# Kernel optimization log

Measured on AMD Instinct MI355X. Metric: run time of the kernel, lower is better.

Reference implementation:

```python
import jax, jax.numpy as jnp
import numpy as np

TEMPERATURE = 0.1
NORMALIZED = True


def _l2norm(x, eps=1e-12):
    # matches F.normalize(p=2, dim=1)
    n = jnp.sqrt(jnp.sum(x * x, axis=1, keepdims=True))
    return x / jnp.maximum(n, eps)


def setup_inputs() -> dict:
    key = jax.random.key(0)
    k1, k2, k3, k4 = jax.random.split(key, 4)
    B, D = 4096, 256
    return {
        "hs": jax.random.normal(k1, (B, D), dtype=jnp.float32),
        "ht0": jax.random.normal(k2, (B, D), dtype=jnp.float32),
        "ht1": jax.random.normal(k3, (B, D), dtype=jnp.float32),
        "labels": jax.random.randint(k4, (B,), 0, 100, dtype=jnp.int64)
        if jax.config.jax_enable_x64 else jax.random.randint(k4, (B,), 0, 100, dtype=jnp.int32),
        "num_views": 2,
    }


def _per_teacher_loss(hs_n, ht_n, mask, logits_mask, batch_size, num_views):
    # features: [N, D] with N = 2B
    features = jnp.concatenate([hs_n, ht_n], axis=0)
    sim = jnp.matmul(features, features.T) / TEMPERATURE          # [N, N]
    exp_logits = jnp.exp(sim) * logits_mask                        # [N, N]
    log_prob = sim - jnp.log(jnp.sum(exp_logits, axis=1, keepdims=True))
    per_inst = -jnp.sum(mask * log_prob, axis=1) / jnp.sum(mask, axis=1)  # [N]
    if num_views > 1:
        per_inst = per_inst.reshape(batch_size, num_views).mean(axis=1)
    return per_inst.mean()


def reference(hs, ht0, ht1, labels, num_views):
    batch_size = labels.shape[0]
    hs = hs.reshape(batch_size, -1)
    ht_list = [ht0.reshape(batch_size, -1), ht1.reshape(batch_size, -1)]
    if NORMALIZED:
        hs = _l2norm(hs)
        ht_list = [_l2norm(ht) for ht in ht_list]

    labels2 = jnp.concatenate([labels, labels])                    # [N]
    mask = (labels2[:, None] == labels2[None, :]).astype(jnp.float32)
    N = 2 * batch_size
    logits_mask = 1.0 - jnp.eye(N, dtype=jnp.float32)              # zero diagonal
    mask = mask * logits_mask

    inter_loss = 0.0
    for ht in ht_list:
        inter_loss = inter_loss + _per_teacher_loss(
            hs, ht, mask, logits_mask, batch_size, num_views)
    return inter_loss / len(ht_list)
```

## Files before the change

### kernel.cpp

```cpp
#include <hip/hip_runtime.h>
#include <hip/hip_bf16.h>

#define B_SIZE 4096
#define D_SIZE 256
#define N_SIZE 8192
#define NCHUNK 8
#define CHUNK (N_SIZE / NCHUNK)
#define GROUP 64
#define NGROUPS (CHUNK / GROUP)

typedef __attribute__((ext_vector_type(8))) short short8;
typedef __attribute__((ext_vector_type(4))) float floatx4;


__device__ __forceinline__ void async16(void* lds, const void* g) {
    __builtin_amdgcn_global_load_lds(
        (const __attribute__((address_space(1))) unsigned int*)g,
        (__attribute__((address_space(3))) unsigned int*)lds, 16, 0, 0);
}
__device__ __forceinline__ void async4(void* lds, const void* g) {
    __builtin_amdgcn_global_load_lds(
        (const __attribute__((address_space(1))) unsigned int*)g,
        (__attribute__((address_space(3))) unsigned int*)lds, 4, 0, 0);
}

__global__ void norm_kernel(const float* __restrict__ hs,
                            const float* __restrict__ ht0,
                            const float* __restrict__ ht1,
                            __hip_bfloat16* __restrict__ dst,
                            float* __restrict__ zero_region) {
    int id  = blockIdx.x;
    int tid = threadIdx.x;
    int gid = id * 256 + tid;
    if (gid < 2 * 2 * N_SIZE) zero_region[gid] = 0.0f;

    const float* src = (id < 4096) ? (hs + id * D_SIZE)
                     : (id < 8192) ? (ht0 + (id - 4096) * D_SIZE)
                                   : (ht1 + (id - 8192) * D_SIZE);
    float x = src[tid];
    float ss = x * x;
#pragma unroll
    for (int off = 32; off > 0; off >>= 1) ss += __shfl_xor(ss, off);
    __shared__ float wsum[4];
    int wave = tid >> 6, lane = tid & 63;
    if (lane == 0) wsum[wave] = ss;
    __syncthreads();
    float tot = wsum[0] + wsum[1] + wsum[2] + wsum[3];
    float inv = 1.0f / fmaxf(sqrtf(tot), 1e-12f);
    dst[id * D_SIZE + tid] = __float2bfloat16(x * inv);
}

__global__ __launch_bounds__(256)
void sim_kernel(const __hip_bfloat16* __restrict__ featS,
                const __hip_bfloat16* __restrict__ featT0,
                const __hip_bfloat16* __restrict__ featT1,
                const int* __restrict__ labels,
                float* __restrict__ Sarr,
                float* __restrict__ Aarr) {
    __shared__ __align__(16) unsigned char sB[2][32768];
    __shared__ int sLab[2][GROUP];

    const int rb    = blockIdx.x;
    const int t     = blockIdx.y;
    const int chunk = blockIdx.z;
    const __hip_bfloat16* featT = t ? featT1 : featT0;

    const int tid  = threadIdx.x;
    const int w    = tid >> 6;
    const int l    = tid & 63;
    const int quad = l >> 4;
    const int lcol = l & 15;
    const int row_base = rb * 128 + w * 32;

    short8 af[2][8];
#pragma unroll
    for (int rt = 0; rt < 2; ++rt) {
        int arow = row_base + rt * 16 + lcol;
        const __hip_bfloat16* ap = (arow < B_SIZE) ? featS + arow * D_SIZE
                                                   : featT + (arow - B_SIZE) * D_SIZE;
#pragma unroll
        for (int ks = 0; ks < 8; ++ks)
            af[rt][ks] = *reinterpret_cast<const short8*>(ap + ks * 32 + quad * 8);
    }

    int labr[2][4];
#pragma unroll
    for (int rt = 0; rt < 2; ++rt)
#pragma unroll
        for (int r = 0; r < 4; ++r)
            labr[rt][r] = labels[(row_base + rt * 16 + quad * 4 + r) & (B_SIZE - 1)];

    float Sp[2][4] = {{0.f,0.f,0.f,0.f},{0.f,0.f,0.f,0.f}};
    float Ap[2][4] = {{0.f,0.f,0.f,0.f},{0.f,0.f,0.f,0.f}};

    const int col0 = chunk * CHUNK;

    auto stage = [&](int b, int cb) {
#pragma unroll
        for (int i = 0; i < 8; ++i) {
            int cl  = i * 2 + (l >> 5);
            int c   = (l & 31) ^ (cl & 7);
            int col = cb + w * 16 + cl;
            const __hip_bfloat16* cp = (col < B_SIZE) ? featS + col * D_SIZE
                                                      : featT + (col - B_SIZE) * D_SIZE;
            async16(&sB[b][w * 8192 + i * 1024], (const char*)cp + c * 16);
        }
        if (w == 0) async4(&sLab[b][0], &labels[(cb + l) & (B_SIZE - 1)]);
    };

    stage(0, col0);

    for (int g = 0; g < NGROUPS; ++g) {
        const int buf = g & 1;
        const int cb  = col0 + g * GROUP;
        __syncthreads();
        if (g + 1 < NGROUPS) stage(buf ^ 1, cb + GROUP);

        floatx4 acc[4][2];
#pragma unroll
        for (int u = 0; u < 4; ++u)
#pragma unroll
            for (int rt = 0; rt < 2; ++rt)
                acc[u][rt] = floatx4{0.f, 0.f, 0.f, 0.f};

#pragma unroll
        for (int ks = 0; ks < 8; ++ks) {
            short8 bf[4];
#pragma unroll
            for (int u = 0; u < 4; ++u)
                bf[u] = *reinterpret_cast<const short8*>(
                    &sB[buf][u * 8192 + lcol * 512 + ((ks * 4 + quad) ^ (lcol & 7)) * 16]);
#pragma unroll
            for (int u = 0; u < 4; ++u)
#pragma unroll
                for (int rt = 0; rt < 2; ++rt)
                    acc[u][rt] = __builtin_amdgcn_mfma_f32_16x16x32_bf16(
                        af[rt][ks], bf[u], acc[u][rt], 0, 0, 0);
        }

#pragma unroll
        for (int u = 0; u < 4; ++u) {
            const int bcol = cb + u * 16 + lcol;
            const int labj = sLab[buf][u * 16 + lcol];
#pragma unroll
            for (int rt = 0; rt < 2; ++rt)
#pragma unroll
                for (int r = 0; r < 4; ++r) {
                    const int row = row_base + rt * 16 + quad * 4 + r;
                    const float a = acc[u][rt][r];
                    const float e = __expf(a * 10.0f);
                    const bool diag = (row == bcol);
                    Sp[rt][r] += diag ? 0.f : e;
                    Ap[rt][r] += (!diag && labj == labr[rt][r]) ? a : 0.f;
                }
        }
    }

#pragma unroll
    for (int rt = 0; rt < 2; ++rt)
#pragma unroll
        for (int r = 0; r < 4; ++r) {
#pragma unroll
            for (int m = 1; m < 16; m <<= 1) {
                Sp[rt][r] += __shfl_xor(Sp[rt][r], m);
                Ap[rt][r] += __shfl_xor(Ap[rt][r], m);
            }
        }
    if (lcol == 0) {
#pragma unroll
        for (int rt = 0; rt < 2; ++rt)
#pragma unroll
            for (int r = 0; r < 4; ++r) {
                const int row = row_base + rt * 16 + quad * 4 + r;
                atomicAdd(&Sarr[t * N_SIZE + row], Sp[rt][r]);
                atomicAdd(&Aarr[t * N_SIZE + row], Ap[rt][r]);
            }
    }
}

__global__ void final_kernel(const float* __restrict__ Sarr,
                             const float* __restrict__ Aarr,
                             const int* __restrict__ labels,
                             float* __restrict__ out) {
    __shared__ int h[128];
    __shared__ float wsum[16];
    int tid = threadIdx.x;
    if (tid < 128) h[tid] = 0;
    __syncthreads();
    for (int i = tid; i < B_SIZE; i += 1024) atomicAdd(&h[labels[i] & 127], 1);
    __syncthreads();
    float acc = 0.f;
    for (int idx = tid; idx < 2 * N_SIZE; idx += 1024) {
        int i = idx & (N_SIZE - 1);
        float M = 2.0f * (float)h[labels[i & (B_SIZE - 1)] & 127] - 1.0f;
        acc += logf(Sarr[idx]) - 10.0f * Aarr[idx] / M;
    }
#pragma unroll
    for (int off = 32; off > 0; off >>= 1) acc += __shfl_xor(acc, off);
    int wv = tid >> 6, ln = tid & 63;
    if (ln == 0) wsum[wv] = acc;
    __syncthreads();
    if (tid == 0) {
        float tot = 0.f;
#pragma unroll
        for (int k = 0; k < 16; ++k) tot += wsum[k];
        out[0] = tot / 16384.0f;
    }
}

extern "C" void kernel_launch(void* const* d_in, const int* in_sizes, int n_in,
                              void* d_out, int out_size, void* d_ws, size_t ws_size,
                              hipStream_t stream) {
    const float* hs     = (const float*)d_in[0];
    const float* ht0    = (const float*)d_in[1];
    const float* ht1    = (const float*)d_in[2];
    const int*   labels = (const int*)d_in[3];

    char* ws = (char*)d_ws;
    float* Sarr = (float*)(ws);
    float* Aarr = (float*)(ws + 65536);
    __hip_bfloat16* featS  = (__hip_bfloat16*)(ws + 131072);
    __hip_bfloat16* featT0 = (__hip_bfloat16*)(ws + 131072 + 2097152);
    __hip_bfloat16* featT1 = (__hip_bfloat16*)(ws + 131072 + 2 * 2097152);

    norm_kernel<<<3 * 4096, 256, 0, stream>>>(hs, ht0, ht1, featS, Sarr);
    sim_kernel<<<dim3(64, 2, NCHUNK), 256, 0, stream>>>(featS, featT0, featT1, labels, Sarr, Aarr);
    final_kernel<<<1, 1024, 0, stream>>>(Sarr, Aarr, labels, (float*)d_out);
}
```

Baseline: 170.2 us.

## Compute positive-pair sums via per-label centroids and drop masking from sim loop

The sim kernel no longer evaluates label and diagonal masks per element. It sums exp over all columns, and a new rowstat kernel subtracts the diagonal term exp(10*|f_i|^2). The masked positive-logit sum is rewritten algebraically as a dot product of each row with per-label feature sums, which a new gvec kernel accumulates with atomics. The sim tile also grows to 64 rows per wave with fewer blocks (launch bounds 2), the LDS layout drops the swizzle, and the final reduction becomes a multi-block ticket pattern. Risks include precision loss from subtracting the diagonal exp out of S, bank conflicts from the unswizzled LDS reads, and the serial per-block gvec reduction.

After: 304.4 us. 1.79x slower.

```diff
diff --git a/kernel.cpp b/kernel.cpp
--- a/kernel.cpp
+++ b/kernel.cpp
@@ -5,11 +5,13 @@
 #define D_SIZE 256
 #define N_SIZE 8192
 #define NCHUNK 8
-#define CHUNK (N_SIZE / NCHUNK)
+#define CHUNK 1024
 #define GROUP 64
 #define NGROUPS (CHUNK / GROUP)
+#define LOG2E10 14.4269504089f
 
 typedef __attribute__((ext_vector_type(8))) short short8;
+typedef __attribute__((ext_vector_type(4))) short short4v;
 typedef __attribute__((ext_vector_type(4))) float floatx4;
 
 
@@ -17,11 +19,6 @@
     __builtin_amdgcn_global_load_lds(
         (const __attribute__((address_space(1))) unsigned int*)g,
         (__attribute__((address_space(3))) unsigned int*)lds, 16, 0, 0);
-}
-__device__ __forceinline__ void async4(void* lds, const void* g) {
-    __builtin_amdgcn_global_load_lds(
-        (const __attribute__((address_space(1))) unsigned int*)g,
-        (__attribute__((address_space(3))) unsigned int*)lds, 4, 0, 0);
 }
 
 __global__ void norm_kernel(const float* __restrict__ hs,
@@ -32,7 +29,7 @@
     int id  = blockIdx.x;
     int tid = threadIdx.x;
     int gid = id * 256 + tid;
-    if (gid < 2 * 2 * N_SIZE) zero_region[gid] = 0.0f;
+    if (gid < 114818) zero_region[gid] = 0.0f;
 
     const float* src = (id < 4096) ? (hs + id * D_SIZE)
                      : (id < 8192) ? (ht0 + (id - 4096) * D_SIZE)
@@ -50,15 +47,44 @@
     dst[id * D_SIZE + tid] = __float2bfloat16(x * inv);
 }
 
-__global__ __launch_bounds__(256)
+__global__ void gvec_kernel(const __hip_bfloat16* __restrict__ featBase,
+                            const int* __restrict__ labels,
+                            float* __restrict__ gOut,
+                            int* __restrict__ cnt) {
+    __shared__ float lg[64 * 256];
+    __shared__ int slab[256];
+    const int b   = blockIdx.x;
+    const int tid = threadIdx.x;
+    const int set = b >> 4;
+    const int rs0 = (b & 15) * 256;
+    const __hip_bfloat16* f = featBase + set * B_SIZE * D_SIZE;
+    float* gset = gOut + set * 32768;
+
+    slab[tid] = labels[rs0 + tid] & 127;
+    __syncthreads();
+    if (set == 0) atomicAdd(&cnt[slab[tid]], 1);
+
+    for (int pass = 0; pass < 2; ++pass) {
+        for (int k = 0; k < 64; ++k) lg[k * 256 + tid] = 0.0f;
+        __syncthreads();
+        for (int it = 0; it < 256; ++it) {
+            int lab = slab[it];
+            if ((lab >> 6) == pass)
+                lg[(lab & 63) * 256 + tid] += __bfloat162float(f[(rs0 + it) * D_SIZE + tid]);
+        }
+        __syncthreads();
+        for (int k = 0; k < 64; ++k)
+            atomicAdd(&gset[pass * 16384 + k * 256 + tid], lg[k * 256 + tid]);
+        __syncthreads();
+    }
+}
+
+__global__ __launch_bounds__(256, 2)
 void sim_kernel(const __hip_bfloat16* __restrict__ featS,
                 const __hip_bfloat16* __restrict__ featT0,
                 const __hip_bfloat16* __restrict__ featT1,
-                const int* __restrict__ labels,
-                float* __restrict__ Sarr,
-                float* __restrict__ Aarr) {
+                float* __restrict__ Sarr) {
     __shared__ __align__(16) unsigned char sB[2][32768];
-    __shared__ int sLab[2][GROUP];
 
     const int rb    = blockIdx.x;
     const int t     = blockIdx.y;
@@ -70,11 +96,11 @@
     const int l    = tid & 63;
     const int quad = l >> 4;
     const int lcol = l & 15;
-    const int row_base = rb * 128 + w * 32;
-
-    short8 af[2][8];
-#pragma unroll
-    for (int rt = 0; rt < 2; ++rt) {
+    const int row_base = rb * 256 + w * 64;
+
+    short8 af[4][8];
+#pragma unroll
+    for (int rt = 0; rt < 4; ++rt) {
         int arow = row_base + rt * 16 + lcol;
         const __hip_bfloat16* ap = (arow < B_SIZE) ? featS + arow * D_SIZE
                                                    : featT + (arow - B_SIZE) * D_SIZE;
@@ -83,128 +109,142 @@
             af[rt][ks] = *reinterpret_cast<const short8*>(ap + ks * 32 + quad * 8);
     }
 
-    int labr[2][4];
-#pragma unroll
-    for (int rt = 0; rt < 2; ++rt)
-#pragma unroll
-        for (int r = 0; r < 4; ++r)
-            labr[rt][r] = labels[(row_base + rt * 16 + quad * 4 + r) & (B_SIZE - 1)];
-
-    float Sp[2][4] = {{0.f,0.f,0.f,0.f},{0.f,0.f,0.f,0.f}};
-    float Ap[2][4] = {{0.f,0.f,0.f,0.f},{0.f,0.f,0.f,0.f}};
+    float Sp[4][4];
+#pragma unroll
+    for (int rt = 0; rt < 4; ++rt)
+#pragma unroll
+        for (int r = 0; r < 4; ++r) Sp[rt][r] = 0.0f;
 
     const int col0 = chunk * CHUNK;
 
     auto stage = [&](int b, int cb) {
-#pragma unroll
-        for (int i = 0; i < 8; ++i) {
-            int cl  = i * 2 + (l >> 5);
-            int c   = (l & 31) ^ (cl & 7);
-            int col = cb + w * 16 + cl;
-            const __hip_bfloat16* cp = (col < B_SIZE) ? featS + col * D_SIZE
-                                                      : featT + (col - B_SIZE) * D_SIZE;
-            async16(&sB[b][w * 8192 + i * 1024], (const char*)cp + c * 16);
-        }
-        if (w == 0) async4(&sLab[b][0], &labels[(cb + l) & (B_SIZE - 1)]);
+        int tb = cb + w * 16;
+        const __hip_bfloat16* cp = (tb < B_SIZE) ? featS + tb * D_SIZE
+                                                 : featT + (tb - B_SIZE) * D_SIZE;
+        const char* gp = (const char*)cp + (l & 15) * 512 + (l >> 4) * 16;
+        unsigned char* lp = &sB[b][w * 8192];
+#pragma unroll
+        for (int ks = 0; ks < 8; ++ks)
+            async16(lp + ks * 1024, gp + ks * 64);
     };
 
     stage(0, col0);
 
     for (int g = 0; g < NGROUPS; ++g) {
         const int buf = g & 1;
-        const int cb  = col0 + g * GROUP;
-        __syncthreads();
-        if (g + 1 < NGROUPS) stage(buf ^ 1, cb + GROUP);
-
-        floatx4 acc[4][2];
-#pragma unroll
-        for (int u = 0; u < 4; ++u)
-#pragma unroll
-            for (int rt = 0; rt < 2; ++rt)
-                acc[u][rt] = floatx4{0.f, 0.f, 0.f, 0.f};
-
-#pragma unroll
-        for (int ks = 0; ks < 8; ++ks) {
-            short8 bf[4];
-#pragma unroll
-            for (int u = 0; u < 4; ++u)
-                bf[u] = *reinterpret_cast<const short8*>(
-                    &sB[buf][u * 8192 + lcol * 512 + ((ks * 4 + quad) ^ (lcol & 7)) * 16]);
-#pragma unroll
-            for (int u = 0; u < 4; ++u)
-#pragma unroll
-                for (int rt = 0; rt < 2; ++rt)
-                    acc[u][rt] = __builtin_amdgcn_mfma_f32_16x16x32_bf16(
-                        af[rt][ks], bf[u], acc[u][rt], 0, 0, 0);
-        }
-
-#pragma unroll
-        for (int u = 0; u < 4; ++u) {
-            const int bcol = cb + u * 16 + lcol;
-            const int labj = sLab[buf][u * 16 + lcol];
-#pragma unroll
-            for (int rt = 0; rt < 2; ++rt)
-#pragma unroll
-                for (int r = 0; r < 4; ++r) {
-                    const int row = row_base + rt * 16 + quad * 4 + r;
-                    const float a = acc[u][rt][r];
-                    const float e = __expf(a * 10.0f);
-                    const bool diag = (row == bcol);
-                    Sp[rt][r] += diag ? 0.f : e;
-                    Ap[rt][r] += (!diag && labj == labr[rt][r]) ? a : 0.f;
-                }
-        }
-    }
-
-#pragma unroll
-    for (int rt = 0; rt < 2; ++rt)
+        __syncthreads();
+        if (g + 1 < NGROUPS) stage(buf ^ 1, col0 + (g + 1) * GROUP);
+
+#pragma unroll
+        for (int up = 0; up < 2; ++up) {
+            floatx4 acc[2][4];
+#pragma unroll
+            for (int j = 0; j < 2; ++j)
+#pragma unroll
+                for (int rt = 0; rt < 4; ++rt) acc[j][rt] = floatx4{0.f, 0.f, 0.f, 0.f};
+
+#pragma unroll
+            for (int ks = 0; ks < 8; ++ks) {
+                short8 bf[2];
+#pragma unroll
+                for (int j = 0; j < 2; ++j)
+                    bf[j] = *reinterpret_cast<const short8*>(
+                        &sB[buf][(up * 2 + j) * 8192 + ks * 1024 + l * 16]);
+#pragma unroll
+                for (int j = 0; j < 2; ++j)
+#pragma unroll
+                    for (int rt = 0; rt < 4; ++rt)
+                        acc[j][rt] = __builtin_amdgcn_mfma_f32_16x16x32_bf16(
+                            af[rt][ks], bf[j], acc[j][rt], 0, 0, 0);
+            }
+#pragma unroll
+            for (int j = 0; j < 2; ++j)
+#pragma unroll
+                for (int rt = 0; rt < 4; ++rt)
+#pragma unroll
+                    for (int r = 0; r < 4; ++r)
+                        Sp[rt][r] += exp2f(acc[j][rt][r] * LOG2E10);
+        }
+    }
+
+#pragma unroll
+    for (int rt = 0; rt < 4; ++rt)
 #pragma unroll
         for (int r = 0; r < 4; ++r) {
 #pragma unroll
-            for (int m = 1; m < 16; m <<= 1) {
-                Sp[rt][r] += __shfl_xor(Sp[rt][r], m);
-                Ap[rt][r] += __shfl_xor(Ap[rt][r], m);
+            for (int m = 1; m < 16; m <<= 1) Sp[rt][r] += __shfl_xor(Sp[rt][r], m);
+        }
+    if (lcol == 0) {
+#pragma unroll
+        for (int rt = 0; rt < 4; ++rt)
+#pragma unroll
+            for (int r = 0; r < 4; ++r) {
+                int row = row_base + rt * 16 + quad * 4 + r;
+                atomicAdd(&Sarr[t * N_SIZE + row], Sp[rt][r]);
             }
-        }
-    if (lcol == 0) {
-#pragma unroll
-        for (int rt = 0; rt < 2; ++rt)
-#pragma unroll
-            for (int r = 0; r < 4; ++r) {
-                const int row = row_base + rt * 16 + quad * 4 + r;
-                atomicAdd(&Sarr[t * N_SIZE + row], Sp[rt][r]);
-                atomicAdd(&Aarr[t * N_SIZE + row], Ap[rt][r]);
-            }
-    }
-}
-
-__global__ void final_kernel(const float* __restrict__ Sarr,
-                             const float* __restrict__ Aarr,
-                             const int* __restrict__ labels,
-                             float* __restrict__ out) {
-    __shared__ int h[128];
-    __shared__ float wsum[16];
-    int tid = threadIdx.x;
-    if (tid < 128) h[tid] = 0;
-    __syncthreads();
-    for (int i = tid; i < B_SIZE; i += 1024) atomicAdd(&h[labels[i] & 127], 1);
-    __syncthreads();
-    float acc = 0.f;
-    for (int idx = tid; idx < 2 * N_SIZE; idx += 1024) {
-        int i = idx & (N_SIZE - 1);
-        float M = 2.0f * (float)h[labels[i & (B_SIZE - 1)] & 127] - 1.0f;
-        acc += logf(Sarr[idx]) - 10.0f * Aarr[idx] / M;
-    }
-#pragma unroll
-    for (int off = 32; off > 0; off >>= 1) acc += __shfl_xor(acc, off);
-    int wv = tid >> 6, ln = tid & 63;
-    if (ln == 0) wsum[wv] = acc;
+    }
+}
+
+__global__ void rowstat_kernel(const __hip_bfloat16* __restrict__ featS,
+                               const __hip_bfloat16* __restrict__ featT0,
+                               const __hip_bfloat16* __restrict__ featT1,
+                               const int* __restrict__ labels,
+                               const float* __restrict__ gAll,
+                               const int* __restrict__ cnt,
+                               const float* __restrict__ Sarr,
+                               float* __restrict__ lossAcc,
+                               int* __restrict__ ticket,
+                               float* __restrict__ out) {
+    __shared__ float wpart[4];
+    const int tid = threadIdx.x;
+    const int wv  = tid >> 6;
+    const int l   = tid & 63;
+    const int waveid = blockIdx.x * 4 + wv;
+    float psum = 0.0f;
+
+    for (int it = 0; it < 64; ++it) {
+        int R = waveid * 64 + it;
+        int t = R >> 13;
+        int i = R & (N_SIZE - 1);
+        const __hip_bfloat16* f = (i < B_SIZE) ? featS + i * D_SIZE
+                                : (t ? featT1 : featT0) + (i - B_SIZE) * D_SIZE;
+        int lab = labels[i & (B_SIZE - 1)] & 127;
+        short4v fb = *reinterpret_cast<const short4v*>(f + l * 4);
+        float fx[4];
+#pragma unroll
+        for (int k = 0; k < 4; ++k) {
+            unsigned int u = ((unsigned int)(unsigned short)fb[k]) << 16;
+            fx[k] = __uint_as_float(u);
+        }
+        const float* gS = gAll + lab * 256 + l * 4;
+        const float* gT = gAll + (1 + t) * 32768 + lab * 256 + l * 4;
+        float dot = 0.f, aii = 0.f;
+#pragma unroll
+        for (int k = 0; k < 4; ++k) {
+            dot += fx[k] * (gS[k] + gT[k]);
+            aii += fx[k] * fx[k];
+        }
+#pragma unroll
+        for (int m = 1; m < 64; m <<= 1) {
+            dot += __shfl_xor(dot, m);
+            aii += __shfl_xor(aii, m);
+        }
+        if (l == 0) {
+            float S = Sarr[t * N_SIZE + i];
+            float M = 2.0f * (float)cnt[lab] - 1.0f;
+            float E = exp2f(LOG2E10 * aii);
+            psum += logf(S - E) - 10.0f * (dot - aii) / M;
+        }
+    }
+    if (l == 0) wpart[wv] = psum;
     __syncthreads();
     if (tid == 0) {
-        float tot = 0.f;
-#pragma unroll
-        for (int k = 0; k < 16; ++k) tot += wsum[k];
-        out[0] = tot / 16384.0f;
+        atomicAdd(lossAcc, wpart[0] + wpart[1] + wpart[2] + wpart[3]);
+        __threadfence();
+        if (atomicAdd(ticket, 1) == 63) {
+            float tot = atomicAdd(lossAcc, 0.0f);
+            out[0] = tot / 16384.0f;
+        }
     }
 }
 
@@ -217,13 +257,18 @@
     const int*   labels = (const int*)d_in[3];
 
     char* ws = (char*)d_ws;
-    float* Sarr = (float*)(ws);
-    float* Aarr = (float*)(ws + 65536);
-    __hip_bfloat16* featS  = (__hip_bfloat16*)(ws + 131072);
-    __hip_bfloat16* featT0 = (__hip_bfloat16*)(ws + 131072 + 2097152);
-    __hip_bfloat16* featT1 = (__hip_bfloat16*)(ws + 131072 + 2 * 2097152);
-
-    norm_kernel<<<3 * 4096, 256, 0, stream>>>(hs, ht0, ht1, featS, Sarr);
-    sim_kernel<<<dim3(64, 2, NCHUNK), 256, 0, stream>>>(featS, featT0, featT1, labels, Sarr, Aarr);
-    final_kernel<<<1, 1024, 0, stream>>>(Sarr, Aarr, labels, (float*)d_out);
-}
+    float* Sarr    = (float*)(ws);
+    float* gAll    = (float*)(ws + 65536);
+    int*   cnt     = (int*)(ws + 458752);
+    float* lossAcc = (float*)(ws + 459264);
+    int*   ticket  = (int*)(ws + 459268);
+    __hip_bfloat16* featS  = (__hip_bfloat16*)(ws + 524288);
+    __hip_bfloat16* featT0 = (__hip_bfloat16*)(ws + 524288 + 2097152);
+    __hip_bfloat16* featT1 = (__hip_bfloat16*)(ws + 524288 + 2 * 2097152);
+
+    norm_kernel<<<3 * 4096, 256, 0, stream>>>(hs, ht0, ht1, featS, (float*)ws);
+    gvec_kernel<<<48, 256, 0, stream>>>(featS, labels, gAll, cnt);
+    sim_kernel<<<dim3(32, 2, NCHUNK), 256, 0, stream>>>(featS, featT0, featT1, Sarr);
+    rowstat_kernel<<<64, 256, 0, stream>>>(featS, featT0, featT1, labels, gAll, cnt,
+                                           Sarr, lossAcc, ticket, (float*)d_out);
+}
```
